# Performance work log

Hardware: AMD Instinct MI355X
Metric: run time of the kernel (lower is better)

## Reference

```python
import jax, jax.numpy as jnp
import numpy as np

EMB = 1024
HEADS = 16
HEAD_DIM = EMB // HEADS
HID = 4096
B, L = 1, 4096
EPS = 1e-5


def _layernorm(x, g, b):
    mu = jnp.mean(x, axis=-1, keepdims=True)
    var = jnp.mean(jnp.square(x - mu), axis=-1, keepdims=True)
    return (x - mu) * jax.lax.rsqrt(var + EPS) * g + b


def setup_inputs() -> dict:
    key = jax.random.key(0)
    ks = jax.random.split(key, 12)
    s = 0.02
    d = {
        "x": jax.random.normal(ks[0], (B, L, EMB), jnp.float32),
        "mask": jnp.ones((1, 1, L, L), jnp.int32),
        "Wq": jax.random.normal(ks[1], (EMB, EMB), jnp.float32) * s,
        "bq": jnp.zeros((EMB,), jnp.float32),
        "Wk": jax.random.normal(ks[2], (EMB, EMB), jnp.float32) * s,
        "bk": jnp.zeros((EMB,), jnp.float32),
        "Wv": jax.random.normal(ks[3], (EMB, EMB), jnp.float32) * s,
        "bv": jnp.zeros((EMB,), jnp.float32),
        "Wo": jax.random.normal(ks[4], (EMB, EMB), jnp.float32) * s,
        "bo": jnp.zeros((EMB,), jnp.float32),
        "g1": jnp.ones((EMB,), jnp.float32),
        "b1": jnp.zeros((EMB,), jnp.float32),
        "W1": jax.random.normal(ks[5], (EMB, HID), jnp.float32) * s,
        "bf1": jnp.zeros((HID,), jnp.float32),
        "W2": jax.random.normal(ks[6], (HID, EMB), jnp.float32) * s,
        "bf2": jnp.zeros((EMB,), jnp.float32),
        "g2": jnp.ones((EMB,), jnp.float32),
        "b2": jnp.zeros((EMB,), jnp.float32),
    }
    return d


def reference(x, mask, Wq, bq, Wk, bk, Wv, bv, Wo, bo, g1, b1, W1, bf1, W2, bf2, g2, b2):
    Bb, Ll, _ = x.shape
    # projections -> [B, H, L, Dh]
    def split(h):
        return h.reshape(Bb, Ll, HEADS, HEAD_DIM).transpose(0, 2, 1, 3)
    Q = split(x @ Wq + bq)
    K = split(x @ Wk + bk)
    V = split(x @ Wv + bv)
    scores = jnp.einsum("bhqd,bhkd->bhqk", Q, K) / jnp.sqrt(jnp.float32(HEAD_DIM))
    scores = jnp.where(mask == 0, jnp.float32(-1e9), scores)
    attn = jax.nn.softmax(scores, axis=-1)
    ctx = jnp.einsum("bhqk,bhkd->bhqd", attn, V)
    ctx = ctx.transpose(0, 2, 1, 3).reshape(Bb, Ll, EMB)
    attn_out = ctx @ Wo + bo
    x = _layernorm(x + attn_out, g1, b1)
    h = jax.nn.gelu(x @ W1 + bf1, approximate=False)
    ffn = h @ W2 + bf2
    x = _layernorm(x + ffn, g2, b2)
    return x
```

## Files before the change

kernel.cpp:

```cpp
#include <hip/hip_runtime.h>
#include <cstdint>
#include <cstddef>

#define EMB   1024
#define SEQ   4096
#define NHEAD 16
#define DHEAD 64
#define HIDD  4096
#define QSTR  2048

typedef float          f32x4 __attribute__((ext_vector_type(4)));
typedef short          s16x8 __attribute__((ext_vector_type(8)));
typedef unsigned short u16x4 __attribute__((ext_vector_type(4)));
typedef unsigned int   u32x2 __attribute__((ext_vector_type(2)));
typedef unsigned short u16;

__device__ __forceinline__ u16 f2bf(float f) {
  unsigned int u = __float_as_uint(f);
  u = u + 0x7FFFu + ((u >> 16) & 1u);
  return (u16)(u >> 16);
}

__device__ __forceinline__ float exp2_hw(float x) {
  return __builtin_amdgcn_exp2f(x);
}

__device__ __forceinline__ void gload16(const void* g, void* l) {
  __builtin_amdgcn_global_load_lds((const __attribute__((address_space(1))) void*)g,
                                   (__attribute__((address_space(3))) void*)l,
                                   16, 0, 0);
}

__global__ __launch_bounds__(256) void cvt_bf16_k(const float* __restrict__ in,
                                                  u16* __restrict__ out, int n4) {
  int idx = blockIdx.x * 256 + threadIdx.x;
  if (idx >= n4) return;
  f32x4 v = ((const f32x4*)in)[idx];
  u16x4 o;
#pragma unroll
  for (int r = 0; r < 4; ++r) o[r] = f2bf(v[r]);
  ((u16x4*)out)[idx] = o;
}

__global__ __launch_bounds__(256) void transpose_bf16_k(const float* __restrict__ in,
                                                        u16* __restrict__ out,
                                                        int K, int N) {
  __shared__ float tile[32][33];
  int n0 = blockIdx.x * 32, k0 = blockIdx.y * 32;
  for (int i = threadIdx.x; i < 1024; i += 256) {
    int r = i >> 5, c = i & 31;
    tile[r][c] = in[(size_t)(k0 + r) * N + n0 + c];
  }
  __syncthreads();
  for (int i = threadIdx.x; i < 1024; i += 256) {
    int r = i >> 5, c = i & 31;
    out[(size_t)(n0 + r) * K + k0 + c] = f2bf(tile[c][r]);
  }
}

__global__ __launch_bounds__(256) void transpose4_bf16_k(const float* __restrict__ W0,
                                                         const float* __restrict__ W1,
                                                         const float* __restrict__ W2,
                                                         const float* __restrict__ W3,
                                                         u16* __restrict__ outbase) {
  __shared__ float tile[32][33];
  int z = blockIdx.z;
  const float* in = (z == 0) ? W0 : (z == 1) ? W1 : (z == 2) ? W2 : W3;
  u16* out = outbase + (size_t)z * EMB * EMB;
  int n0 = blockIdx.x * 32, k0 = blockIdx.y * 32;
  for (int i = threadIdx.x; i < 1024; i += 256) {
    int r = i >> 5, c = i & 31;
    tile[r][c] = in[(size_t)(k0 + r) * EMB + n0 + c];
  }
  __syncthreads();
  for (int i = threadIdx.x; i < 1024; i += 256) {
    int r = i >> 5, c = i & 31;
    out[(size_t)(n0 + r) * EMB + k0 + c] = f2bf(tile[c][r]);
  }
}

template <int MODE>
__global__ __launch_bounds__(512, 4) void gemm_bt_k(const u16* __restrict__ A,
                                                    const u16* __restrict__ Bt,
                                                    const float* __restrict__ bias,
                                                    const float* __restrict__ res,
                                                    void* __restrict__ Out,
                                                    int M, int N, int K) {
  __shared__ __align__(16) u16 As[2][128 * 32];
  __shared__ __align__(16) u16 Bs[2][128 * 32];
  int t = threadIdx.x, lane = t & 63, w = t >> 6;
  int wm = w >> 2, wn = w & 3;
  int m0 = blockIdx.y * 128, n0 = blockIdx.x * 128;
  int lr = lane & 15, lg = lane >> 4, lk = lg << 3;
  int srow = t >> 2;
  int scol = (t & 3) << 3;

  const u16* gA = A  + (size_t)(m0 + srow) * K + scol;
  const u16* gB = Bt + (size_t)(n0 + srow) * K + scol;

  f32x4 acc[4][2];
#pragma unroll
  for (int i = 0; i < 4; ++i)
#pragma unroll
    for (int j = 0; j < 2; ++j)
#pragma unroll
      for (int r = 0; r < 4; ++r) acc[i][j][r] = 0.f;

  gload16(gA, (char*)As[0] + (w << 10));
  gload16(gB, (char*)Bs[0] + (w << 10));

  int cur = 0;
  for (int k0 = 0; k0 < K; k0 += 32, cur ^= 1) {
    __syncthreads();
    if (k0 + 32 < K) {
      int kn = k0 + 32;
      gload16(gA + kn, (char*)As[cur ^ 1] + (w << 10));
      gload16(gB + kn, (char*)Bs[cur ^ 1] + (w << 10));
    }

    s16x8 af[4], bf[2];
#pragma unroll
    for (int i = 0; i < 4; ++i)
      af[i] = *(const s16x8*)&As[cur][(wm * 64 + i * 16 + lr) * 32 + lk];
#pragma unroll
    for (int j = 0; j < 2; ++j)
      bf[j] = *(const s16x8*)&Bs[cur][(wn * 32 + j * 16 + lr) * 32 + lk];
#pragma unroll
    for (int i = 0; i < 4; ++i)
#pragma unroll
      for (int j = 0; j < 2; ++j)
        acc[i][j] = __builtin_amdgcn_mfma_f32_16x16x32_bf16(af[i], bf[j], acc[i][j], 0, 0, 0);
  }

  int orow0 = m0 + wm * 64, ocol0 = n0 + wn * 32;
#pragma unroll
  for (int i = 0; i < 4; ++i)
#pragma unroll
    for (int j = 0; j < 2; ++j) {
      int col = ocol0 + j * 16 + lr;
      float bcol;
      if (MODE == 3)      bcol = 0.f;
      else if (MODE == 4) bcol = (col < 1024) ? bias[col] : res[col - 1024];
      else                bcol = bias[col];
#pragma unroll
      for (int r = 0; r < 4; ++r) {
        int row = orow0 + i * 16 + lg * 4 + r;
        size_t idx = (size_t)row * N + col;
        if (MODE == 0) {
          ((u16*)Out)[idx] = f2bf(acc[i][j][r] + bcol);
        } else if (MODE == 1) {
          ((float*)Out)[idx] = acc[i][j][r] + bcol + res[idx];
        } else if (MODE == 2) {
          float v = acc[i][j][r] + bcol;
          float gl = 0.5f * v * (1.f + erff(v * 0.70710678118654752f));
          ((u16*)Out)[idx] = f2bf(gl);
        } else if (MODE == 3) {
          ((u16*)Out)[idx] = f2bf(acc[i][j][r] + bias[row]);
        } else {
          float v = acc[i][j][r] + bcol;
          ((u16*)Out)[idx] = f2bf(col < 1024 ? v * 0.18033688011112042f : v);
        }
      }
    }
}

__global__ __launch_bounds__(512) void attn_k(const u16* __restrict__ Qb,
                                              const u16* __restrict__ Kb,
                                              const u16* __restrict__ Vt,
                                              u16* __restrict__ ctx) {
  __shared__ __align__(16) u16 Ks[2][64 * 64];
  __shared__ __align__(16) u16 Vs[2][64 * 64];
  int t = threadIdx.x, lane = t & 63, w = t >> 6;
  int b = blockIdx.x;
  int xcd = b & 7, slot = b >> 3;
  int h = 2 * xcd + (slot >> 5);
  int q0 = (slot & 31) * 128 + w * 16;
  int lr = lane & 15, lg = lane >> 4, lk = lg << 3;
  int swl = (lr & 7) << 4;

  int srw = w * 8 + (lane >> 3);
  int ssb = ((lane & 7) << 4) ^ ((lane >> 3) << 4);
  const u16* gK0 = Kb + (size_t)srw * QSTR + h * DHEAD + (ssb >> 1);
  const u16* gV0 = Vt + (size_t)(h * DHEAD + srw) * SEQ + (ssb >> 1);
  int dstb = w << 10;

  s16x8 aq[2];
#pragma unroll
  for (int kf = 0; kf < 2; ++kf)
    aq[kf] = *(const s16x8*)&Qb[(size_t)(q0 + lr) * QSTR + h * DHEAD + kf * 32 + lk];

  f32x4 o[4];
#pragma unroll
  for (int dj = 0; dj < 4; ++dj)
#pragma unroll
    for (int r = 0; r < 4; ++r) o[dj][r] = 0.f;
  float m_run = -3.0e38f, l_run = 0.f;

  gload16(gK0, (char*)Ks[0] + dstb);
  gload16(gV0, (char*)Vs[0] + dstb);
  __syncthreads();

  int cur = 0;
  for (int kb = 0; kb < SEQ; kb += 64) {
    if (kb + 64 < SEQ) {
      size_t ko = (size_t)(kb + 64);
      gload16(gK0 + ko * QSTR, (char*)Ks[cur ^ 1] + dstb);
      gload16(gV0 + ko,        (char*)Vs[cur ^ 1] + dstb);
    }
    const char* Kc = (const char*)Ks[cur];
    const char* Vc = (const char*)Vs[cur];

    f32x4 st[4];
#pragma unroll
    for (int nj = 0; nj < 4; ++nj) {
#pragma unroll
      for (int r = 0; r < 4; ++r) st[nj][r] = 0.f;
      int rowb = (nj * 16 + lr) * 128;
#pragma unroll
      for (int kf = 0; kf < 2; ++kf) {
        s16x8 bk = *(const s16x8*)(Kc + rowb + ((kf * 64 + lg * 16) ^ swl));
        st[nj] = __builtin_amdgcn_mfma_f32_16x16x32_bf16(bk, aq[kf], st[nj], 0, 0, 0);
      }
    }

    float mx = st[0][0];
#pragma unroll
    for (int nj = 0; nj < 4; ++nj)
#pragma unroll
      for (int r = 0; r < 4; ++r) mx = fmaxf(mx, st[nj][r]);
    mx = fmaxf(mx, __shfl_xor(mx, 16));
    mx = fmaxf(mx, __shfl_xor(mx, 32));
    if (!__all(mx - m_run <= 8.f)) {
      float mn = fmaxf(m_run, mx);
      float fac = exp2_hw(m_run - mn);
      m_run = mn;
      l_run *= fac;
      float fq[4];
#pragma unroll
      for (int r = 0; r < 4; ++r) fq[r] = __shfl(fac, lg * 4 + r);
#pragma unroll
      for (int dj = 0; dj < 4; ++dj)
#pragma unroll
        for (int r = 0; r < 4; ++r) o[dj][r] *= fq[r];
    }
    float rsum = 0.f;
#pragma unroll
    for (int nj = 0; nj < 4; ++nj)
#pragma unroll
      for (int r = 0; r < 4; ++r) {
        float p = exp2_hw(st[nj][r] - m_run);
        st[nj][r] = p;
        rsum += p;
      }
    rsum += __shfl_xor(rsum, 16);
    rsum += __shfl_xor(rsum, 32);
    l_run += rsum;

    u32x2 pk[4];
#pragma unroll
    for (int nj = 0; nj < 4; ++nj) {
      unsigned int lo, hi;
      asm("v_cvt_pk_bf16_f32 %0, %1, %2" : "=v"(lo) : "v"(st[nj][0]), "v"(st[nj][1]));
      asm("v_cvt_pk_bf16_f32 %0, %1, %2" : "=v"(hi) : "v"(st[nj][2]), "v"(st[nj][3]));
      pk[nj][0] = lo; pk[nj][1] = hi;
    }

#pragma unroll
    for (int dj = 0; dj < 4; ++dj) {
      int rowb = (dj * 16 + lr) * 128;
#pragma unroll
      for (int nj = 0; nj < 4; ++nj) {
        u32x2 vb = *(const u32x2*)(Vc + rowb + ((nj * 32 + lg * 8) ^ swl));
        asm volatile("s_nop 1\n\tv_mfma_f32_16x16x16_bf16 %0, %1, %2, %0"
                     : "+v"(o[dj]) : "v"(pk[nj]), "v"(vb));
      }
    }

    __syncthreads();
    cur ^= 1;
  }

  float linv = 1.f / l_run;
  float lq[4];
#pragma unroll
  for (int r = 0; r < 4; ++r) lq[r] = __shfl(linv, lg * 4 + r);
#pragma unroll
  for (int dj = 0; dj < 4; ++dj)
#pragma unroll
    for (int r = 0; r < 4; ++r)
      ctx[(size_t)(q0 + lg * 4 + r) * EMB + h * DHEAD + dj * 16 + lr] =
          f2bf(o[dj][r] * lq[r]);
}

__global__ __launch_bounds__(256) void ln_k(const float* __restrict__ hin,
                                            const float* __restrict__ g,
                                            const float* __restrict__ be,
                                            float* __restrict__ outf,
                                            u16* __restrict__ outb) {
  int row = blockIdx.x, t = threadIdx.x;
  int lane = t & 63, w = t >> 6;
  f32x4 v = ((const f32x4*)(hin + (size_t)row * EMB))[t];
  float s  = v[0] + v[1] + v[2] + v[3];
  float s2 = v[0] * v[0] + v[1] * v[1] + v[2] * v[2] + v[3] * v[3];
#pragma unroll
  for (int m = 1; m < 64; m <<= 1) { s += __shfl_xor(s, m); s2 += __shfl_xor(s2, m); }
  __shared__ float red[8];
  if (lane == 0) { red[w] = s; red[4 + w] = s2; }
  __syncthreads();
  s  = red[0] + red[1] + red[2] + red[3];
  s2 = red[4] + red[5] + red[6] + red[7];
  float mu  = s * (1.f / EMB);
  float var = s2 * (1.f / EMB) - mu * mu;
  float rs  = rsqrtf(var + 1e-5f);
  f32x4 gv = ((const f32x4*)g)[t];
  f32x4 bv = ((const f32x4*)be)[t];
  f32x4 y;
#pragma unroll
  for (int r = 0; r < 4; ++r) y[r] = (v[r] - mu) * rs * gv[r] + bv[r];
  if (outf) ((f32x4*)(outf + (size_t)row * EMB))[t] = y;
  if (outb) {
    u16x4 ob;
#pragma unroll
    for (int r = 0; r < 4; ++r) ob[r] = f2bf(y[r]);
    ((u16x4*)(outb + (size_t)row * EMB))[t] = ob;
  }
}

extern "C" void kernel_launch(void* const* d_in, const int* in_sizes, int n_in,
                              void* d_out, int out_size, void* d_ws, size_t ws_size,
                              hipStream_t stream) {
  const float* x  = (const float*)d_in[0];
  const float* Wq = (const float*)d_in[2];
  const float* bq = (const float*)d_in[3];
  const float* Wk = (const float*)d_in[4];
  const float* bk = (const float*)d_in[5];
  const float* Wv = (const float*)d_in[6];
  const float* bv = (const float*)d_in[7];
  const float* Wo = (const float*)d_in[8];
  const float* bo = (const float*)d_in[9];
  const float* g1 = (const float*)d_in[10];
  const float* b1 = (const float*)d_in[11];
  const float* W1 = (const float*)d_in[12];
  const float* bf1 = (const float*)d_in[13];
  const float* W2 = (const float*)d_in[14];
  const float* bf2 = (const float*)d_in[15];
  const float* g2 = (const float*)d_in[16];
  const float* b2 = (const float*)d_in[17];

  char* ws = (char*)d_ws;
  const size_t MB = (size_t)1 << 20;
  u16*   wqt = (u16*)(ws + 0 * MB);
  u16*   wvt = (u16*)(ws + 4 * MB);
  u16*   wot = (u16*)(ws + 6 * MB);
  u16*   w1t = (u16*)(ws + 8 * MB);
  u16*   w2t = (u16*)(ws + 16 * MB);
  u16*   xb  = (u16*)(ws + 24 * MB);
  u16*   QKb = (u16*)(ws + 32 * MB);
  u16*   VtG = (u16*)(ws + 48 * MB);
  u16*   ctx = (u16*)(ws + 56 * MB);
  float* h1  = (float*)(ws + 64 * MB);
  float* x1  = (float*)(ws + 80 * MB);
  u16*   x1b = (u16*)(ws + 96 * MB);
  u16*   hid = (u16*)(ws + 32 * MB);
  float* h2  = (float*)(ws + 64 * MB);

  cvt_bf16_k<<<dim3(SEQ * EMB / 4 / 256), 256, 0, stream>>>(x, xb, SEQ * EMB / 4);
  transpose4_bf16_k<<<dim3(EMB / 32, EMB / 32, 4), 256, 0, stream>>>(Wq, Wk, Wv, Wo, wqt);
  transpose_bf16_k<<<dim3(HIDD / 32, EMB / 32), 256, 0, stream>>>(W1, w1t, EMB, HIDD);
  transpose_bf16_k<<<dim3(EMB / 32, HIDD / 32), 256, 0, stream>>>(W2, w2t, HIDD, EMB);

  gemm_bt_k<4><<<dim3(QSTR / 128, SEQ / 128), 512, 0, stream>>>(xb, wqt, bq, bk, QKb, SEQ, QSTR, EMB);
  gemm_bt_k<3><<<dim3(SEQ / 128, EMB / 128), 512, 0, stream>>>(wvt, xb, bv, nullptr, VtG, EMB, SEQ, EMB);

  attn_k<<<dim3(512), 512, 0, stream>>>(QKb, QKb + 1024, VtG, ctx);

  gemm_bt_k<1><<<dim3(EMB / 128, SEQ / 128), 512, 0, stream>>>(ctx, wot, bo, x, h1, SEQ, EMB, EMB);
  ln_k<<<dim3(SEQ), 256, 0, stream>>>(h1, g1, b1, x1, x1b);
  gemm_bt_k<2><<<dim3(HIDD / 128, SEQ / 128), 512, 0, stream>>>(x1b, w1t, bf1, nullptr, hid, SEQ, HIDD, EMB);
  gemm_bt_k<1><<<dim3(EMB / 128, SEQ / 128), 512, 0, stream>>>(hid, w2t, bf2, x1, h2, SEQ, EMB, HIDD);
  ln_k<<<dim3(SEQ), 256, 0, stream>>>(h2, g2, b2, (float*)d_out, nullptr);
}
```

Baseline: 349.2 us.

## Triple-buffer attention K/V and software-pipeline QK^T; add BN=64 GEMM tiles

The attention kernel moves to three LDS buffers for K and V and computes the next tile's QK^T scores before running softmax and PV on the current tile. This lets matrix-core work overlap the exp/max math and hides global-load latency better. Separately, the GEMM kernel gains a BN template parameter, and the N=1024 GEMMs (V projection, Wo, W2) use 128x64 tiles to double the block count. In exchange, the GEMMs load A twice as often per output, and attention uses more LDS and registers.

```diff
diff --git a/kernel.cpp b/kernel.cpp
--- a/kernel.cpp
+++ b/kernel.cpp
@@ -79,35 +79,39 @@
   }
 }
 
-template <int MODE>
+template <int MODE, int BN>
 __global__ __launch_bounds__(512, 4) void gemm_bt_k(const u16* __restrict__ A,
                                                     const u16* __restrict__ Bt,
                                                     const float* __restrict__ bias,
                                                     const float* __restrict__ res,
                                                     void* __restrict__ Out,
                                                     int M, int N, int K) {
+  constexpr int AI  = (BN == 128) ? 4 : 2;
+  constexpr int MST = (BN == 128) ? 64 : 32;
   __shared__ __align__(16) u16 As[2][128 * 32];
-  __shared__ __align__(16) u16 Bs[2][128 * 32];
+  __shared__ __align__(16) u16 Bs[2][BN * 32];
   int t = threadIdx.x, lane = t & 63, w = t >> 6;
-  int wm = w >> 2, wn = w & 3;
-  int m0 = blockIdx.y * 128, n0 = blockIdx.x * 128;
+  int wm = (BN == 128) ? (w >> 2) : (w >> 1);
+  int wn = (BN == 128) ? (w & 3) : (w & 1);
+  int m0 = blockIdx.y * 128, n0 = blockIdx.x * BN;
   int lr = lane & 15, lg = lane >> 4, lk = lg << 3;
   int srow = t >> 2;
   int scol = (t & 3) << 3;
+  bool doB = (BN == 128) || (w < 4);
 
   const u16* gA = A  + (size_t)(m0 + srow) * K + scol;
-  const u16* gB = Bt + (size_t)(n0 + srow) * K + scol;
-
-  f32x4 acc[4][2];
-#pragma unroll
-  for (int i = 0; i < 4; ++i)
+  const u16* gB = Bt + (size_t)(n0 + (srow & (BN - 1))) * K + scol;
+
+  f32x4 acc[AI][2];
+#pragma unroll
+  for (int i = 0; i < AI; ++i)
 #pragma unroll
     for (int j = 0; j < 2; ++j)
 #pragma unroll
       for (int r = 0; r < 4; ++r) acc[i][j][r] = 0.f;
 
   gload16(gA, (char*)As[0] + (w << 10));
-  gload16(gB, (char*)Bs[0] + (w << 10));
+  if (doB) gload16(gB, (char*)Bs[0] + (w << 10));
 
   int cur = 0;
   for (int k0 = 0; k0 < K; k0 += 32, cur ^= 1) {
@@ -115,26 +119,26 @@
     if (k0 + 32 < K) {
       int kn = k0 + 32;
       gload16(gA + kn, (char*)As[cur ^ 1] + (w << 10));
-      gload16(gB + kn, (char*)Bs[cur ^ 1] + (w << 10));
-    }
-
-    s16x8 af[4], bf[2];
-#pragma unroll
-    for (int i = 0; i < 4; ++i)
-      af[i] = *(const s16x8*)&As[cur][(wm * 64 + i * 16 + lr) * 32 + lk];
+      if (doB) gload16(gB + kn, (char*)Bs[cur ^ 1] + (w << 10));
+    }
+
+    s16x8 af[AI], bf[2];
+#pragma unroll
+    for (int i = 0; i < AI; ++i)
+      af[i] = *(const s16x8*)&As[cur][(wm * MST + i * 16 + lr) * 32 + lk];
 #pragma unroll
     for (int j = 0; j < 2; ++j)
       bf[j] = *(const s16x8*)&Bs[cur][(wn * 32 + j * 16 + lr) * 32 + lk];
 #pragma unroll
-    for (int i = 0; i < 4; ++i)
+    for (int i = 0; i < AI; ++i)
 #pragma unroll
       for (int j = 0; j < 2; ++j)
         acc[i][j] = __builtin_amdgcn_mfma_f32_16x16x32_bf16(af[i], bf[j], acc[i][j], 0, 0, 0);
   }
 
-  int orow0 = m0 + wm * 64, ocol0 = n0 + wn * 32;
-#pragma unroll
-  for (int i = 0; i < 4; ++i)
+  int orow0 = m0 + wm * MST, ocol0 = n0 + wn * 32;
+#pragma unroll
+  for (int i = 0; i < AI; ++i)
 #pragma unroll
     for (int j = 0; j < 2; ++j) {
       int col = ocol0 + j * 16 + lr;
@@ -168,8 +172,8 @@
                                               const u16* __restrict__ Kb,
                                               const u16* __restrict__ Vt,
                                               u16* __restrict__ ctx) {
-  __shared__ __align__(16) u16 Ks[2][64 * 64];
-  __shared__ __align__(16) u16 Vs[2][64 * 64];
+  __shared__ __align__(16) u16 Ks[3][64 * 64];
+  __shared__ __align__(16) u16 Vs[3][64 * 64];
   int t = threadIdx.x, lane = t & 63, w = t >> 6;
   int b = blockIdx.x;
   int xcd = b & 7, slot = b >> 3;
@@ -178,8 +182,8 @@
   int lr = lane & 15, lg = lane >> 4, lk = lg << 3;
   int swl = (lr & 7) << 4;
 
+  int ssb = ((lane & 7) << 4) ^ ((lane >> 3) << 4);
   int srw = w * 8 + (lane >> 3);
-  int ssb = ((lane & 7) << 4) ^ ((lane >> 3) << 4);
   const u16* gK0 = Kb + (size_t)srw * QSTR + h * DHEAD + (ssb >> 1);
   const u16* gV0 = Vt + (size_t)(h * DHEAD + srw) * SEQ + (ssb >> 1);
   int dstb = w << 10;
@@ -200,29 +204,47 @@
   gload16(gV0, (char*)Vs[0] + dstb);
   __syncthreads();
 
-  int cur = 0;
-  for (int kb = 0; kb < SEQ; kb += 64) {
-    if (kb + 64 < SEQ) {
-      size_t ko = (size_t)(kb + 64);
-      gload16(gK0 + ko * QSTR, (char*)Ks[cur ^ 1] + dstb);
-      gload16(gV0 + ko,        (char*)Vs[cur ^ 1] + dstb);
-    }
-    const char* Kc = (const char*)Ks[cur];
-    const char* Vc = (const char*)Vs[cur];
-
-    f32x4 st[4];
+  f32x4 stA[4], stB[4];
+  {
+    const char* Kc = (const char*)Ks[0];
 #pragma unroll
     for (int nj = 0; nj < 4; ++nj) {
 #pragma unroll
-      for (int r = 0; r < 4; ++r) st[nj][r] = 0.f;
+      for (int r = 0; r < 4; ++r) stA[nj][r] = 0.f;
       int rowb = (nj * 16 + lr) * 128;
 #pragma unroll
       for (int kf = 0; kf < 2; ++kf) {
         s16x8 bk = *(const s16x8*)(Kc + rowb + ((kf * 64 + lg * 16) ^ swl));
-        st[nj] = __builtin_amdgcn_mfma_f32_16x16x32_bf16(bk, aq[kf], st[nj], 0, 0, 0);
+        stA[nj] = __builtin_amdgcn_mfma_f32_16x16x32_bf16(bk, aq[kf], stA[nj], 0, 0, 0);
       }
     }
-
+  }
+  gload16(gK0 + (size_t)64 * QSTR, (char*)Ks[1] + dstb);
+  gload16(gV0 + 64,                (char*)Vs[1] + dstb);
+
+  int bc = 0, b1 = 1, b2 = 2;
+
+  auto step = [&](int tt, f32x4 (&st)[4], f32x4 (&stN)[4]) {
+    __syncthreads();
+    if (tt + 2 < 64) {
+      size_t ko = (size_t)(tt + 2) * 64;
+      gload16(gK0 + ko * QSTR, (char*)Ks[0] + b2 * 8192 + dstb);
+      gload16(gV0 + ko,        (char*)Vs[0] + b2 * 8192 + dstb);
+    }
+    if (tt + 1 < 64) {
+      const char* Kc = (const char*)Ks[0] + b1 * 8192;
+#pragma unroll
+      for (int nj = 0; nj < 4; ++nj) {
+#pragma unroll
+        for (int r = 0; r < 4; ++r) stN[nj][r] = 0.f;
+        int rowb = (nj * 16 + lr) * 128;
+#pragma unroll
+        for (int kf = 0; kf < 2; ++kf) {
+          s16x8 bk = *(const s16x8*)(Kc + rowb + ((kf * 64 + lg * 16) ^ swl));
+          stN[nj] = __builtin_amdgcn_mfma_f32_16x16x32_bf16(bk, aq[kf], stN[nj], 0, 0, 0);
+        }
+      }
+    }
     float mx = st[0][0];
 #pragma unroll
     for (int nj = 0; nj < 4; ++nj)
@@ -265,6 +287,7 @@
       pk[nj][0] = lo; pk[nj][1] = hi;
     }
 
+    const char* Vc = (const char*)Vs[0] + bc * 8192;
 #pragma unroll
     for (int dj = 0; dj < 4; ++dj) {
       int rowb = (dj * 16 + lr) * 128;
@@ -275,9 +298,12 @@
                      : "+v"(o[dj]) : "v"(pk[nj]), "v"(vb));
       }
     }
-
-    __syncthreads();
-    cur ^= 1;
+    int tmp = bc; bc = b1; b1 = b2; b2 = tmp;
+  };
+
+  for (int tt = 0; tt < 64; tt += 2) {
+    step(tt, stA, stB);
+    step(tt + 1, stB, stA);
   }
 
   float linv = 1.f / l_run;
@@ -369,14 +395,14 @@
   transpose_bf16_k<<<dim3(HIDD / 32, EMB / 32), 256, 0, stream>>>(W1, w1t, EMB, HIDD);
   transpose_bf16_k<<<dim3(EMB / 32, HIDD / 32), 256, 0, stream>>>(W2, w2t, HIDD, EMB);
 
-  gemm_bt_k<4><<<dim3(QSTR / 128, SEQ / 128), 512, 0, stream>>>(xb, wqt, bq, bk, QKb, SEQ, QSTR, EMB);
-  gemm_bt_k<3><<<dim3(SEQ / 128, EMB / 128), 512, 0, stream>>>(wvt, xb, bv, nullptr, VtG, EMB, SEQ, EMB);
+  gemm_bt_k<4, 128><<<dim3(QSTR / 128, SEQ / 128), 512, 0, stream>>>(xb, wqt, bq, bk, QKb, SEQ, QSTR, EMB);
+  gemm_bt_k<3, 64><<<dim3(SEQ / 64, EMB / 128), 512, 0, stream>>>(wvt, xb, bv, nullptr, VtG, EMB, SEQ, EMB);
 
   attn_k<<<dim3(512), 512, 0, stream>>>(QKb, QKb + 1024, VtG, ctx);
 
-  gemm_bt_k<1><<<dim3(EMB / 128, SEQ / 128), 512, 0, stream>>>(ctx, wot, bo, x, h1, SEQ, EMB, EMB);
+  gemm_bt_k<1, 64><<<dim3(EMB / 64, SEQ / 128), 512, 0, stream>>>(ctx, wot, bo, x, h1, SEQ, EMB, EMB);
   ln_k<<<dim3(SEQ), 256, 0, stream>>>(h1, g1, b1, x1, x1b);
-  gemm_bt_k<2><<<dim3(HIDD / 128, SEQ / 128), 512, 0, stream>>>(x1b, w1t, bf1, nullptr, hid, SEQ, HIDD, EMB);
-  gemm_bt_k<1><<<dim3(EMB / 128, SEQ / 128), 512, 0, stream>>>(hid, w2t, bf2, x1, h2, SEQ, EMB, HIDD);
+  gemm_bt_k<2, 128><<<dim3(HIDD / 128, SEQ / 128), 512, 0, stream>>>(x1b, w1t, bf1, nullptr, hid, SEQ, HIDD, EMB);
+  gemm_bt_k<1, 64><<<dim3(EMB / 64, SEQ / 128), 512, 0, stream>>>(hid, w2t, bf2, x1, h2, SEQ, EMB, HIDD);
   ln_k<<<dim3(SEQ), 256, 0, stream>>>(h2, g2, b2, (float*)d_out, nullptr);
 }
```

Result: faster. 336.3 us (-3.7%).
